# Kernel optimization log

Hardware: AMD Instinct MI355X
Metric: run time of the kernel (lower is better)

Reference implementation:

```python
import jax, jax.numpy as jnp
import numpy as np

N = 100000       # nodes
E = 1600000      # edges
D_IN = 128       # input_dim
D_H = 64         # embedding_dim
N_LAYERS = 3     # total GCNConv layers (conv1 + 2 hidden)
DROP_P = 0.5     # F.dropout default (training=True by default in functional form)


def setup_inputs() -> dict:
    key = jax.random.key(0)
    ks = jax.random.split(key, 8)
    x = jax.random.normal(ks[0], (N, D_IN), dtype=jnp.float32)
    edge_index = jax.random.randint(ks[1], (2, E), 0, N, dtype=jnp.int32)
    edge_attr = jax.random.uniform(ks[2], (E,), dtype=jnp.float32)
    # learned parameters (glorot-ish scale, zero bias like PyG defaults)
    W1 = jax.random.normal(ks[3], (D_IN, D_H), dtype=jnp.float32) / np.sqrt(D_IN).astype(np.float32)
    b1 = jnp.zeros((D_H,), jnp.float32)
    Wh = jax.random.normal(ks[4], (N_LAYERS - 1, D_H, D_H), dtype=jnp.float32) / np.sqrt(D_H).astype(np.float32)
    bh = jnp.zeros((N_LAYERS - 1, D_H), jnp.float32)
    lin_W = jax.random.normal(ks[5], (D_H, 1), dtype=jnp.float32) / np.sqrt(D_H).astype(np.float32)
    lin_b = jnp.zeros((1,), jnp.float32)
    return dict(x=x, edge_index=edge_index, edge_attr=edge_attr,
                W1=W1, b1=b1, Wh=Wh, bh=bh, lin_W=lin_W, lin_b=lin_b)


def _gcn_norm(edge_index, edge_weight):
    # PyG gcn_norm: add self-loops with weight 1, symmetric deg^-1/2 normalization.
    loop = jnp.arange(N, dtype=edge_index.dtype)
    src = jnp.concatenate([edge_index[0], loop])   # message sources
    dst = jnp.concatenate([edge_index[1], loop])   # aggregate at targets
    w = jnp.concatenate([edge_weight, jnp.ones((N,), edge_weight.dtype)])
    deg = jax.ops.segment_sum(w, dst, num_segments=N)
    dinv = jnp.where(deg > 0, jax.lax.rsqrt(deg), 0.0)
    norm = dinv[src] * w * dinv[dst]               # [E+N]
    return src, dst, norm


def _gcn_conv(h, W, b, src, dst, norm):
    h = h @ W                                       # [N, D]
    msg = h[src] * norm[:, None]                    # gather + scale, [E+N, D]
    out = jax.ops.segment_sum(msg, dst, num_segments=N)  # scatter-add
    return out + b


def _dropout(h, key, p=DROP_P):
    keep = jax.random.bernoulli(key, 1.0 - p, h.shape)
    return jnp.where(keep, h / (1.0 - p), 0.0)


def reference(x, edge_index, edge_attr, W1, b1, Wh, bh, lin_W, lin_b):
    src, dst, norm = _gcn_norm(edge_index, edge_attr)
    dk = jax.random.split(jax.random.key(42), N_LAYERS)
    h = _dropout(jax.nn.elu(_gcn_conv(x, W1, b1, src, dst, norm)), dk[0])
    for i in range(N_LAYERS - 1):
        h = _dropout(jax.nn.elu(_gcn_conv(h, Wh[i], bh[i], src, dst, norm)), dk[i + 1])
    return h @ lin_W + lin_b                        # [N, 1]
```

## Files before the change

kernel.cpp:

```cpp
#include <hip/hip_runtime.h>
#include <hip/hip_fp16.h>
#include <stdint.h>

#define NNODES 100000
#define NEDGES 1600000
#define DINPUT 128
#define DH 64
#define NELEM (NNODES * DH)
#define CAP 48
#define SCAN_B 1024
#define SCAN_NB ((NNODES + SCAN_B - 1) / SCAN_B)

#define G_GEMM (NNODES / 32)
#define G_EDGE (NEDGES / 256)
#define G_GATH (NNODES / 16)

__host__ __device__ __forceinline__ void tf2x32(uint32_t k0, uint32_t k1,
                                                uint32_t x0, uint32_t x1,
                                                uint32_t* o0, uint32_t* o1) {
  uint32_t k2 = k0 ^ k1 ^ 0x1BD11BDAu;
  x0 += k0; x1 += k1;
#define TF_ROT(r) { x0 += x1; x1 = (x1 << (r)) | (x1 >> (32 - (r))); x1 ^= x0; }
  TF_ROT(13) TF_ROT(15) TF_ROT(26) TF_ROT(6)
  x0 += k1; x1 += k2 + 1u;
  TF_ROT(17) TF_ROT(29) TF_ROT(16) TF_ROT(24)
  x0 += k2; x1 += k0 + 2u;
  TF_ROT(13) TF_ROT(15) TF_ROT(26) TF_ROT(6)
  x0 += k0; x1 += k1 + 3u;
  TF_ROT(17) TF_ROT(29) TF_ROT(16) TF_ROT(24)
  x0 += k1; x1 += k2 + 4u;
  TF_ROT(13) TF_ROT(15) TF_ROT(26) TF_ROT(6)
  x0 += k2; x1 += k0 + 5u;
#undef TF_ROT
  *o0 = x0; *o1 = x1;
}

__device__ __forceinline__ float4 h4_load(const int2* hp, size_t idx) {
  int2 r = hp[idx];
  __half2 a = *reinterpret_cast<__half2*>(&r.x);
  __half2 b = *reinterpret_cast<__half2*>(&r.y);
  float2 fa = __half22float2(a);
  float2 fb = __half22float2(b);
  return float4{fa.x, fa.y, fb.x, fb.y};
}
__device__ __forceinline__ int2 h4_pack(float4 v) {
  __half2 a = __floats2half2_rn(v.x, v.y);
  __half2 b = __floats2half2_rn(v.z, v.w);
  int2 r;
  r.x = *reinterpret_cast<int*>(&a);
  r.y = *reinterpret_cast<int*>(&b);
  return r;
}

__global__ void k_zero(int* cnt) {
  int n = blockIdx.x * 256 + threadIdx.x;
  if (n < NNODES) cnt[n] = 0;
}

__global__ __launch_bounds__(256) void k_fill_gemm(
    const int* __restrict__ src, const int* __restrict__ dst,
    const float* __restrict__ w, int* cnt, int2* __restrict__ cp,
    const float* __restrict__ x, const float* __restrict__ W1,
    __half* __restrict__ B, int gemm_only) {
  __shared__ float Wt[DH][DINPUT + 4];
  __shared__ float4 rows4[32][DINPUT / 4];
  int t = threadIdx.x;
  int bid = blockIdx.x;
  int g, r;
  if (gemm_only) { g = bid; r = 2; } else { g = bid / 3; r = bid % 3; }
  if (r == 2) {
    for (int i = t; i < DINPUT * DH; i += 256) {
      int k = i >> 6, d = i & 63;
      Wt[d][k] = W1[i];
    }
    int n0 = g * 32;
    const float4* hv = (const float4*)x;
    for (int i = t; i < 32 * (DINPUT / 4); i += 256) {
      int rr = i >> 5, kk = i & 31;
      rows4[rr][kk] = hv[(size_t)(n0 + rr) * (DINPUT / 4) + kk];
    }
    __syncthreads();
    int d = t & 63;
    int wv = t >> 6;
    float acc[8] = {0.f, 0.f, 0.f, 0.f, 0.f, 0.f, 0.f, 0.f};
    const float4* wt4 = (const float4*)&Wt[d][0];
#pragma unroll 4
    for (int kq = 0; kq < DINPUT / 4; ++kq) {
      float4 wq = wt4[kq];
#pragma unroll
      for (int rr = 0; rr < 8; ++rr) {
        float4 hq = rows4[wv * 8 + rr][kq];
        acc[rr] += hq.x * wq.x + hq.y * wq.y + hq.z * wq.z + hq.w * wq.w;
      }
    }
#pragma unroll
    for (int rr = 0; rr < 8; ++rr)
      B[(size_t)(n0 + wv * 8 + rr) * DH + d] = __float2half_rn(acc[rr]);
  } else {
    int f = g * 2 + r;
    int e = f * 256 + t;
    int s = src[e], d = dst[e];
    int slot = atomicAdd(&cnt[d], 1);
    if (slot < CAP) cp[(size_t)d * CAP + slot] = int2{s, __float_as_int(w[e])};
  }
}

__global__ void k_hist(const int* __restrict__ dst, int* cnt) {
  int e = blockIdx.x * 256 + threadIdx.x;
  if (e < NEDGES) atomicAdd(&cnt[dst[e]], 1);
}

__global__ __launch_bounds__(1024) void k_scan1(const int* __restrict__ cnt,
                                                int* __restrict__ lpre,
                                                int* __restrict__ bsum) {
  __shared__ int ps[SCAN_B];
  int t = threadIdx.x;
  int n = blockIdx.x * SCAN_B + t;
  int v = (n < NNODES) ? cnt[n] : 0;
  ps[t] = v;
  __syncthreads();
  for (int off = 1; off < SCAN_B; off <<= 1) {
    int u = (t >= off) ? ps[t - off] : 0;
    __syncthreads();
    ps[t] += u;
    __syncthreads();
  }
  if (n < NNODES) lpre[n] = ps[t] - v;
  if (t == SCAN_B - 1) bsum[blockIdx.x] = ps[t];
}

__global__ __launch_bounds__(128) void k_scan2(int* bsum) {
  __shared__ int ps[128];
  int t = threadIdx.x;
  int v = (t < SCAN_NB) ? bsum[t] : 0;
  ps[t] = v;
  __syncthreads();
  for (int off = 1; off < 128; off <<= 1) {
    int u = (t >= off) ? ps[t - off] : 0;
    __syncthreads();
    ps[t] += u;
    __syncthreads();
  }
  if (t < SCAN_NB) bsum[t] = ps[t] - v;
}

__global__ __launch_bounds__(1024) void k_scan3(const int* __restrict__ bsum,
                                                int* __restrict__ lpre_rowptr,
                                                int* __restrict__ wptr) {
  int t = threadIdx.x;
  int n = blockIdx.x * SCAN_B + t;
  if (n < NNODES) {
    int r = lpre_rowptr[n] + bsum[blockIdx.x];
    lpre_rowptr[n] = r;
    wptr[n] = r;
  }
  if (n == 0) lpre_rowptr[NNODES] = NEDGES;
}

__global__ void k_fill_compact(const int* __restrict__ src, const int* __restrict__ dst,
                               const float* __restrict__ w, int* wptr,
                               int2* __restrict__ cp) {
  int e = blockIdx.x * 256 + threadIdx.x;
  if (e < NEDGES) {
    int s = src[e], d = dst[e];
    int slot = atomicAdd(&wptr[d], 1);
    cp[slot] = int2{s, __float_as_int(w[e])};
  }
}

template <int PADDED>
__global__ __launch_bounds__(256) void k_degrow(const int* __restrict__ rowptr,
                                                const int* __restrict__ cnt,
                                                const int2* __restrict__ cp,
                                                float* __restrict__ dinv) {
  int g = blockIdx.x * 16 + (threadIdx.x >> 4);
  int sl = threadIdx.x & 15;
  int beg = PADDED ? g * CAP : rowptr[g];
  int num = PADDED ? min(cnt[g], CAP) : rowptr[g + 1] - beg;
  float s = 0.0f;
  for (int i = sl; i < num; i += 16) s += __int_as_float(cp[beg + i].y);
  s += __shfl_xor(s, 1);
  s += __shfl_xor(s, 2);
  s += __shfl_xor(s, 4);
  s += __shfl_xor(s, 8);
  if (sl == 0) dinv[g] = 1.0f / sqrtf(1.0f + s);
}

template <int MODE, int PADDED>
__global__ __launch_bounds__(256) void k_gg(
    const __half* __restrict__ h2, const int* __restrict__ rowptr,
    const int* __restrict__ cnt, const int2* __restrict__ cpair,
    const float* __restrict__ dinv, const float* __restrict__ bias,
    const float* __restrict__ Wn, const float* __restrict__ lw,
    const float* __restrict__ lb, void* __restrict__ outp,
    uint32_t k0, uint32_t k1) {
  __shared__ float4 Ws4[DH * 16];
  __shared__ float4 hs4[16 * 17];
  int t = threadIdx.x;
  int g = blockIdx.x * 16 + (t >> 4);
  int sl = t & 15;
  int n = t >> 4;
  const int2* h4 = (const int2*)h2;

  if (MODE == 0) {
    const float4* wv = (const float4*)Wn;
    for (int i = t; i < DH * 16; i += 256) Ws4[i] = wv[i];
  }

  float dg = dinv[g];
  float4 self = h4_load(h4, (size_t)g * 16 + sl);
  float4 acc = {0.f, 0.f, 0.f, 0.f};

  int beg = PADDED ? g * CAP : rowptr[g];
  int end = beg + (PADDED ? min(cnt[g], CAP) : rowptr[g + 1] - beg);

  int e = beg;
  for (; e + 8 <= end; e += 8) {
    int2 p0 = cpair[e + 0], p1 = cpair[e + 1], p2 = cpair[e + 2], p3 = cpair[e + 3];
    int2 p4 = cpair[e + 4], p5 = cpair[e + 5], p6 = cpair[e + 6], p7 = cpair[e + 7];
    float d0 = dinv[p0.x], d1 = dinv[p1.x], d2 = dinv[p2.x], d3 = dinv[p3.x];
    float d4 = dinv[p4.x], d5 = dinv[p5.x], d6 = dinv[p6.x], d7 = dinv[p7.x];
    float4 v0 = h4_load(h4, (size_t)p0.x * 16 + sl);
    float4 v1 = h4_load(h4, (size_t)p1.x * 16 + sl);
    float4 v2 = h4_load(h4, (size_t)p2.x * 16 + sl);
    float4 v3 = h4_load(h4, (size_t)p3.x * 16 + sl);
    float4 v4 = h4_load(h4, (size_t)p4.x * 16 + sl);
    float4 v5 = h4_load(h4, (size_t)p5.x * 16 + sl);
    float4 v6 = h4_load(h4, (size_t)p6.x * 16 + sl);
    float4 v7 = h4_load(h4, (size_t)p7.x * 16 + sl);
    float w0 = d0 * __int_as_float(p0.y), w1 = d1 * __int_as_float(p1.y);
    float w2 = d2 * __int_as_float(p2.y), w3 = d3 * __int_as_float(p3.y);
    float w4 = d4 * __int_as_float(p4.y), w5 = d5 * __int_as_float(p5.y);
    float w6 = d6 * __int_as_float(p6.y), w7 = d7 * __int_as_float(p7.y);
    acc.x += v0.x * w0 + v1.x * w1 + v2.x * w2 + v3.x * w3
           + v4.x * w4 + v5.x * w5 + v6.x * w6 + v7.x * w7;
    acc.y += v0.y * w0 + v1.y * w1 + v2.y * w2 + v3.y * w3
           + v4.y * w4 + v5.y * w5 + v6.y * w6 + v7.y * w7;
    acc.z += v0.z * w0 + v1.z * w1 + v2.z * w2 + v3.z * w3
           + v4.z * w4 + v5.z * w5 + v6.z * w6 + v7.z * w7;
    acc.w += v0.w * w0 + v1.w * w1 + v2.w * w2 + v3.w * w3
           + v4.w * w4 + v5.w * w5 + v6.w * w6 + v7.w * w7;
  }
  for (; e < end; ++e) {
    int2 p = cpair[e];
    float nm = dinv[p.x] * __int_as_float(p.y);
    float4 v = h4_load(h4, (size_t)p.x * 16 + sl);
    acc.x += v.x * nm;
    acc.y += v.y * nm;
    acc.z += v.z * nm;
    acc.w += v.w * nm;
  }

  const float4 bv = ((const float4*)bias)[sl];
  acc.x = dg * (acc.x + dg * self.x) + bv.x;
  acc.y = dg * (acc.y + dg * self.y) + bv.y;
  acc.z = dg * (acc.z + dg * self.z) + bv.z;
  acc.w = dg * (acc.w + dg * self.w) + bv.w;

  acc.x = (acc.x > 0.0f) ? acc.x : expm1f(acc.x);
  acc.y = (acc.y > 0.0f) ? acc.y : expm1f(acc.y);
  acc.z = (acc.z > 0.0f) ? acc.z : expm1f(acc.z);
  acc.w = (acc.w > 0.0f) ? acc.w : expm1f(acc.w);

  uint32_t base = (uint32_t)g * 64u + (uint32_t)sl * 4u;
  uint32_t o0, o1;
  tf2x32(k0, k1, 0u, base + 0u, &o0, &o1);
  acc.x = (((o0 ^ o1) >> 31) == 0u) ? 2.0f * acc.x : 0.0f;
  tf2x32(k0, k1, 0u, base + 1u, &o0, &o1);
  acc.y = (((o0 ^ o1) >> 31) == 0u) ? 2.0f * acc.y : 0.0f;
  tf2x32(k0, k1, 0u, base + 2u, &o0, &o1);
  acc.z = (((o0 ^ o1) >> 31) == 0u) ? 2.0f * acc.z : 0.0f;
  tf2x32(k0, k1, 0u, base + 3u, &o0, &o1);
  acc.w = (((o0 ^ o1) >> 31) == 0u) ? 2.0f * acc.w : 0.0f;

  if (MODE == 1) {
    const float4 lv = ((const float4*)lw)[sl];
    float dot = acc.x * lv.x + acc.y * lv.y + acc.z * lv.z + acc.w * lv.w;
    dot += __shfl_xor(dot, 1);
    dot += __shfl_xor(dot, 2);
    dot += __shfl_xor(dot, 4);
    dot += __shfl_xor(dot, 8);
    if (sl == 0) ((float*)outp)[g] = dot + lb[0];
  } else {
    hs4[n * 17 + sl] = acc;
    __syncthreads();
    float4 o = {0.f, 0.f, 0.f, 0.f};
#pragma unroll
    for (int dq = 0; dq < 16; ++dq) {
      float4 hq = hs4[n * 17 + dq];
      float4 w0 = Ws4[(dq * 4 + 0) * 16 + sl];
      float4 w1 = Ws4[(dq * 4 + 1) * 16 + sl];
      float4 w2 = Ws4[(dq * 4 + 2) * 16 + sl];
      float4 w3 = Ws4[(dq * 4 + 3) * 16 + sl];
      o.x += hq.x * w0.x + hq.y * w1.x + hq.z * w2.x + hq.w * w3.x;
      o.y += hq.x * w0.y + hq.y * w1.y + hq.z * w2.y + hq.w * w3.y;
      o.z += hq.x * w0.z + hq.y * w1.z + hq.z * w2.z + hq.w * w3.z;
      o.w += hq.x * w0.w + hq.y * w1.w + hq.z * w2.w + hq.w * w3.w;
    }
    ((int2*)outp)[(size_t)g * 16 + sl] = h4_pack(o);
  }
}

extern "C" void kernel_launch(void* const* d_in, const int* in_sizes, int n_in,
                              void* d_out, int out_size, void* d_ws, size_t ws_size,
                              hipStream_t stream) {
  const float* x   = (const float*)d_in[0];
  const int*   ei  = (const int*)d_in[1];
  const float* ew  = (const float*)d_in[2];
  const float* W1  = (const float*)d_in[3];
  const float* b1  = (const float*)d_in[4];
  const float* Wh  = (const float*)d_in[5];
  const float* bh  = (const float*)d_in[6];
  const float* lw  = (const float*)d_in[7];
  const float* lb  = (const float*)d_in[8];
  float* out = (float*)d_out;

  const int* src = ei;
  const int* dst = ei + NEDGES;

  const size_t capE = (size_t)NNODES * CAP;
  const size_t needPadded =
      (size_t)NELEM * 2 * 2 + capE * 8 +
      ((size_t)NNODES * 3 + 1 + SCAN_NB) * 4;
  const bool padded = ws_size >= needPadded;
  const size_t nSlots = padded ? capE : (size_t)NEDGES;

  __half* A     = (__half*)d_ws;
  __half* B     = A + (size_t)NELEM;
  int2*  cpair  = (int2*)(B + (size_t)NELEM);
  float* dinv   = (float*)(cpair + nSlots);
  int*   cnt    = (int*)(dinv + (size_t)NNODES);
  int*   rowptr = cnt + (size_t)NNODES;
  int*   wptr   = rowptr + (size_t)NNODES + 1;
  int*   bsum   = wptr + (size_t)NNODES;

  uint32_t dk[3][2];
  for (uint32_t i = 0; i < 3; ++i) tf2x32(0u, 42u, 0u, i, &dk[i][0], &dk[i][1]);

  const int gN = (NNODES + 255) / 256;
  const float* Wh0 = Wh;
  const float* Wh1 = Wh + (size_t)DH * DH;

  if (padded) {
    k_zero<<<gN, 256, 0, stream>>>(cnt);
    k_fill_gemm<<<3 * G_GEMM, 256, 0, stream>>>(src, dst, ew, cnt, cpair,
                                                x, W1, B, 0);
    k_degrow<1><<<G_GATH, 256, 0, stream>>>(rowptr, cnt, cpair, dinv);

    k_gg<0, 1><<<G_GATH, 256, 0, stream>>>(B, rowptr, cnt, cpair, dinv, b1,
                                           Wh0, lw, lb, A, dk[0][0], dk[0][1]);
    k_gg<0, 1><<<G_GATH, 256, 0, stream>>>(A, rowptr, cnt, cpair, dinv, bh,
                                           Wh1, lw, lb, B, dk[1][0], dk[1][1]);
    k_gg<1, 1><<<G_GATH, 256, 0, stream>>>(B, rowptr, cnt, cpair, dinv, bh + DH,
                                           nullptr, lw, lb, out, dk[2][0], dk[2][1]);
  } else {
    k_zero<<<gN, 256, 0, stream>>>(cnt);
    k_hist<<<G_EDGE, 256, 0, stream>>>(dst, cnt);
    k_scan1<<<SCAN_NB, SCAN_B, 0, stream>>>(cnt, rowptr, bsum);
    k_scan2<<<1, 128, 0, stream>>>(bsum);
    k_scan3<<<SCAN_NB, SCAN_B, 0, stream>>>(bsum, rowptr, wptr);
    k_fill_compact<<<G_EDGE, 256, 0, stream>>>(src, dst, ew, wptr, cpair);
    k_degrow<0><<<G_GATH, 256, 0, stream>>>(rowptr, cnt, cpair, dinv);
    k_fill_gemm<<<G_GEMM, 256, 0, stream>>>(src, dst, ew, cnt, nullptr,
                                            x, W1, B, 1);

    k_gg<0, 0><<<G_GATH, 256, 0, stream>>>(B, rowptr, cnt, cpair, dinv, b1,
                                           Wh0, lw, lb, A, dk[0][0], dk[0][1]);
    k_gg<0, 0><<<G_GATH, 256, 0, stream>>>(A, rowptr, cnt, cpair, dinv, bh,
                                           Wh1, lw, lb, B, dk[1][0], dk[1][1]);
    k_gg<1, 0><<<G_GATH, 256, 0, stream>>>(B, rowptr, cnt, cpair, dinv, bh + DH,
                                           nullptr, lw, lb, out, dk[2][0], dk[2][1]);
  }
}
```

Before: 260.6 us.

## Gather 8 halves per lane with 32 nodes per block; nontemporal edge fill

The gather kernel now assigns 8 lanes per node, each loading 16-byte int4 chunks of fp16 features, so a block processes 32 nodes instead of 16. This halves the grid, and the 64x64 dense transform is remapped so each thread handles two nodes. The fill kernel also uses nontemporal loads for the edge arrays and a nontemporal packed 64-bit store for adjacency pairs. Wider loads cut instruction count per gathered row, but each gathered row is split across fewer lanes and per-thread register use rises.

```diff
diff --git a/kernel.cpp b/kernel.cpp
--- a/kernel.cpp
+++ b/kernel.cpp
@@ -14,6 +14,7 @@
 #define G_GEMM (NNODES / 32)
 #define G_EDGE (NEDGES / 256)
 #define G_GATH (NNODES / 16)
+#define G_GATH2 (NNODES / 32)
 
 __host__ __device__ __forceinline__ void tf2x32(uint32_t k0, uint32_t k1,
                                                 uint32_t x0, uint32_t x1,
@@ -35,13 +36,13 @@
   *o0 = x0; *o1 = x1;
 }
 
-__device__ __forceinline__ float4 h4_load(const int2* hp, size_t idx) {
-  int2 r = hp[idx];
-  __half2 a = *reinterpret_cast<__half2*>(&r.x);
-  __half2 b = *reinterpret_cast<__half2*>(&r.y);
-  float2 fa = __half22float2(a);
-  float2 fb = __half22float2(b);
-  return float4{fa.x, fa.y, fb.x, fb.y};
+__device__ __forceinline__ void h8_unpack(int4 r, float* f) {
+  __half2* h = reinterpret_cast<__half2*>(&r);
+  float2 a;
+  a = __half22float2(h[0]); f[0] = a.x; f[1] = a.y;
+  a = __half22float2(h[1]); f[2] = a.x; f[3] = a.y;
+  a = __half22float2(h[2]); f[4] = a.x; f[5] = a.y;
+  a = __half22float2(h[3]); f[6] = a.x; f[7] = a.y;
 }
 __device__ __forceinline__ int2 h4_pack(float4 v) {
   __half2 a = __floats2half2_rn(v.x, v.y);
@@ -99,9 +100,14 @@
   } else {
     int f = g * 2 + r;
     int e = f * 256 + t;
-    int s = src[e], d = dst[e];
+    int s  = __builtin_nontemporal_load(src + e);
+    int d  = __builtin_nontemporal_load(dst + e);
+    float wv = __builtin_nontemporal_load(w + e);
     int slot = atomicAdd(&cnt[d], 1);
-    if (slot < CAP) cp[(size_t)d * CAP + slot] = int2{s, __float_as_int(w[e])};
+    if (slot < CAP) {
+      long long pv = ((long long)__float_as_int(wv) << 32) | (unsigned)s;
+      __builtin_nontemporal_store(pv, (long long*)(cp + (size_t)d * CAP + slot));
+    }
   }
 }
 
@@ -195,12 +201,12 @@
     const float* __restrict__ lb, void* __restrict__ outp,
     uint32_t k0, uint32_t k1) {
   __shared__ float4 Ws4[DH * 16];
-  __shared__ float4 hs4[16 * 17];
-  int t = threadIdx.x;
-  int g = blockIdx.x * 16 + (t >> 4);
-  int sl = t & 15;
-  int n = t >> 4;
-  const int2* h4 = (const int2*)h2;
+  __shared__ float4 hs4[32 * 17];
+  int t = threadIdx.x;
+  int gl = t >> 3;
+  int g = blockIdx.x * 32 + gl;
+  int sl = t & 7;
+  const int4* h8 = (const int4*)h2;
 
   if (MODE == 0) {
     const float4* wv = (const float4*)Wn;
@@ -208,8 +214,9 @@
   }
 
   float dg = dinv[g];
-  float4 self = h4_load(h4, (size_t)g * 16 + sl);
-  float4 acc = {0.f, 0.f, 0.f, 0.f};
+  float self[8];
+  h8_unpack(h8[(size_t)g * 8 + sl], self);
+  float acc[8] = {0.f, 0.f, 0.f, 0.f, 0.f, 0.f, 0.f, 0.f};
 
   int beg = PADDED ? g * CAP : rowptr[g];
   int end = beg + (PADDED ? min(cnt[g], CAP) : rowptr[g + 1] - beg);
@@ -218,86 +225,83 @@
   for (; e + 8 <= end; e += 8) {
     int2 p0 = cpair[e + 0], p1 = cpair[e + 1], p2 = cpair[e + 2], p3 = cpair[e + 3];
     int2 p4 = cpair[e + 4], p5 = cpair[e + 5], p6 = cpair[e + 6], p7 = cpair[e + 7];
-    float d0 = dinv[p0.x], d1 = dinv[p1.x], d2 = dinv[p2.x], d3 = dinv[p3.x];
-    float d4 = dinv[p4.x], d5 = dinv[p5.x], d6 = dinv[p6.x], d7 = dinv[p7.x];
-    float4 v0 = h4_load(h4, (size_t)p0.x * 16 + sl);
-    float4 v1 = h4_load(h4, (size_t)p1.x * 16 + sl);
-    float4 v2 = h4_load(h4, (size_t)p2.x * 16 + sl);
-    float4 v3 = h4_load(h4, (size_t)p3.x * 16 + sl);
-    float4 v4 = h4_load(h4, (size_t)p4.x * 16 + sl);
-    float4 v5 = h4_load(h4, (size_t)p5.x * 16 + sl);
-    float4 v6 = h4_load(h4, (size_t)p6.x * 16 + sl);
-    float4 v7 = h4_load(h4, (size_t)p7.x * 16 + sl);
-    float w0 = d0 * __int_as_float(p0.y), w1 = d1 * __int_as_float(p1.y);
-    float w2 = d2 * __int_as_float(p2.y), w3 = d3 * __int_as_float(p3.y);
-    float w4 = d4 * __int_as_float(p4.y), w5 = d5 * __int_as_float(p5.y);
-    float w6 = d6 * __int_as_float(p6.y), w7 = d7 * __int_as_float(p7.y);
-    acc.x += v0.x * w0 + v1.x * w1 + v2.x * w2 + v3.x * w3
-           + v4.x * w4 + v5.x * w5 + v6.x * w6 + v7.x * w7;
-    acc.y += v0.y * w0 + v1.y * w1 + v2.y * w2 + v3.y * w3
-           + v4.y * w4 + v5.y * w5 + v6.y * w6 + v7.y * w7;
-    acc.z += v0.z * w0 + v1.z * w1 + v2.z * w2 + v3.z * w3
-           + v4.z * w4 + v5.z * w5 + v6.z * w6 + v7.z * w7;
-    acc.w += v0.w * w0 + v1.w * w1 + v2.w * w2 + v3.w * w3
-           + v4.w * w4 + v5.w * w5 + v6.w * w6 + v7.w * w7;
+    int4 r0 = h8[(size_t)p0.x * 8 + sl];
+    int4 r1 = h8[(size_t)p1.x * 8 + sl];
+    int4 r2 = h8[(size_t)p2.x * 8 + sl];
+    int4 r3 = h8[(size_t)p3.x * 8 + sl];
+    int4 r4 = h8[(size_t)p4.x * 8 + sl];
+    int4 r5 = h8[(size_t)p5.x * 8 + sl];
+    int4 r6 = h8[(size_t)p6.x * 8 + sl];
+    int4 r7 = h8[(size_t)p7.x * 8 + sl];
+    float w0 = dinv[p0.x] * __int_as_float(p0.y);
+    float w1 = dinv[p1.x] * __int_as_float(p1.y);
+    float w2 = dinv[p2.x] * __int_as_float(p2.y);
+    float w3 = dinv[p3.x] * __int_as_float(p3.y);
+    float w4 = dinv[p4.x] * __int_as_float(p4.y);
+    float w5 = dinv[p5.x] * __int_as_float(p5.y);
+    float w6 = dinv[p6.x] * __int_as_float(p6.y);
+    float w7 = dinv[p7.x] * __int_as_float(p7.y);
+    float v[8];
+#define ACC8(R, W) { h8_unpack(R, v); _Pragma("unroll") \
+    for (int j = 0; j < 8; ++j) acc[j] += v[j] * (W); }
+    ACC8(r0, w0) ACC8(r1, w1) ACC8(r2, w2) ACC8(r3, w3)
+    ACC8(r4, w4) ACC8(r5, w5) ACC8(r6, w6) ACC8(r7, w7)
   }
   for (; e < end; ++e) {
     int2 p = cpair[e];
     float nm = dinv[p.x] * __int_as_float(p.y);
-    float4 v = h4_load(h4, (size_t)p.x * 16 + sl);
-    acc.x += v.x * nm;
-    acc.y += v.y * nm;
-    acc.z += v.z * nm;
-    acc.w += v.w * nm;
-  }
-
-  const float4 bv = ((const float4*)bias)[sl];
-  acc.x = dg * (acc.x + dg * self.x) + bv.x;
-  acc.y = dg * (acc.y + dg * self.y) + bv.y;
-  acc.z = dg * (acc.z + dg * self.z) + bv.z;
-  acc.w = dg * (acc.w + dg * self.w) + bv.w;
-
-  acc.x = (acc.x > 0.0f) ? acc.x : expm1f(acc.x);
-  acc.y = (acc.y > 0.0f) ? acc.y : expm1f(acc.y);
-  acc.z = (acc.z > 0.0f) ? acc.z : expm1f(acc.z);
-  acc.w = (acc.w > 0.0f) ? acc.w : expm1f(acc.w);
-
-  uint32_t base = (uint32_t)g * 64u + (uint32_t)sl * 4u;
-  uint32_t o0, o1;
-  tf2x32(k0, k1, 0u, base + 0u, &o0, &o1);
-  acc.x = (((o0 ^ o1) >> 31) == 0u) ? 2.0f * acc.x : 0.0f;
-  tf2x32(k0, k1, 0u, base + 1u, &o0, &o1);
-  acc.y = (((o0 ^ o1) >> 31) == 0u) ? 2.0f * acc.y : 0.0f;
-  tf2x32(k0, k1, 0u, base + 2u, &o0, &o1);
-  acc.z = (((o0 ^ o1) >> 31) == 0u) ? 2.0f * acc.z : 0.0f;
-  tf2x32(k0, k1, 0u, base + 3u, &o0, &o1);
-  acc.w = (((o0 ^ o1) >> 31) == 0u) ? 2.0f * acc.w : 0.0f;
+    float v[8];
+    h8_unpack(h8[(size_t)p.x * 8 + sl], v);
+#pragma unroll
+    for (int j = 0; j < 8; ++j) acc[j] += v[j] * nm;
+  }
+#undef ACC8
+
+  const float4* b4 = (const float4*)bias;
+  float4 ba = b4[sl * 2 + 0], bb = b4[sl * 2 + 1];
+  float bv[8] = {ba.x, ba.y, ba.z, ba.w, bb.x, bb.y, bb.z, bb.w};
+  uint32_t base = (uint32_t)g * 64u + (uint32_t)sl * 8u;
+#pragma unroll
+  for (int j = 0; j < 8; ++j) {
+    float h = dg * (acc[j] + dg * self[j]) + bv[j];
+    h = (h > 0.0f) ? h : expm1f(h);
+    uint32_t o0, o1;
+    tf2x32(k0, k1, 0u, base + (uint32_t)j, &o0, &o1);
+    acc[j] = (((o0 ^ o1) >> 31) == 0u) ? 2.0f * h : 0.0f;
+  }
 
   if (MODE == 1) {
-    const float4 lv = ((const float4*)lw)[sl];
-    float dot = acc.x * lv.x + acc.y * lv.y + acc.z * lv.z + acc.w * lv.w;
+    const float4* l4 = (const float4*)lw;
+    float4 la = l4[sl * 2 + 0], lbv = l4[sl * 2 + 1];
+    float dot = acc[0] * la.x + acc[1] * la.y + acc[2] * la.z + acc[3] * la.w
+              + acc[4] * lbv.x + acc[5] * lbv.y + acc[6] * lbv.z + acc[7] * lbv.w;
     dot += __shfl_xor(dot, 1);
     dot += __shfl_xor(dot, 2);
     dot += __shfl_xor(dot, 4);
-    dot += __shfl_xor(dot, 8);
     if (sl == 0) ((float*)outp)[g] = dot + lb[0];
   } else {
-    hs4[n * 17 + sl] = acc;
-    __syncthreads();
-    float4 o = {0.f, 0.f, 0.f, 0.f};
-#pragma unroll
-    for (int dq = 0; dq < 16; ++dq) {
-      float4 hq = hs4[n * 17 + dq];
-      float4 w0 = Ws4[(dq * 4 + 0) * 16 + sl];
-      float4 w1 = Ws4[(dq * 4 + 1) * 16 + sl];
-      float4 w2 = Ws4[(dq * 4 + 2) * 16 + sl];
-      float4 w3 = Ws4[(dq * 4 + 3) * 16 + sl];
-      o.x += hq.x * w0.x + hq.y * w1.x + hq.z * w2.x + hq.w * w3.x;
-      o.y += hq.x * w0.y + hq.y * w1.y + hq.z * w2.y + hq.w * w3.y;
-      o.z += hq.x * w0.z + hq.y * w1.z + hq.z * w2.z + hq.w * w3.z;
-      o.w += hq.x * w0.w + hq.y * w1.w + hq.z * w2.w + hq.w * w3.w;
-    }
-    ((int2*)outp)[(size_t)g * 16 + sl] = h4_pack(o);
+    hs4[gl * 17 + sl * 2 + 0] = float4{acc[0], acc[1], acc[2], acc[3]};
+    hs4[gl * 17 + sl * 2 + 1] = float4{acc[4], acc[5], acc[6], acc[7]};
+    __syncthreads();
+    int n2 = t >> 4, sl2 = t & 15;
+#pragma unroll
+    for (int it = 0; it < 2; ++it) {
+      int node = n2 + it * 16;
+      float4 o = {0.f, 0.f, 0.f, 0.f};
+#pragma unroll
+      for (int dq = 0; dq < 16; ++dq) {
+        float4 hq = hs4[node * 17 + dq];
+        float4 w0 = Ws4[(dq * 4 + 0) * 16 + sl2];
+        float4 w1 = Ws4[(dq * 4 + 1) * 16 + sl2];
+        float4 w2 = Ws4[(dq * 4 + 2) * 16 + sl2];
+        float4 w3 = Ws4[(dq * 4 + 3) * 16 + sl2];
+        o.x += hq.x * w0.x + hq.y * w1.x + hq.z * w2.x + hq.w * w3.x;
+        o.y += hq.x * w0.y + hq.y * w1.y + hq.z * w2.y + hq.w * w3.y;
+        o.z += hq.x * w0.z + hq.y * w1.z + hq.z * w2.z + hq.w * w3.z;
+        o.w += hq.x * w0.w + hq.y * w1.w + hq.z * w2.w + hq.w * w3.w;
+      }
+      ((int2*)outp)[((size_t)blockIdx.x * 32 + node) * 16 + sl2] = h4_pack(o);
+    }
   }
 }
 
@@ -347,12 +351,12 @@
                                                 x, W1, B, 0);
     k_degrow<1><<<G_GATH, 256, 0, stream>>>(rowptr, cnt, cpair, dinv);
 
-    k_gg<0, 1><<<G_GATH, 256, 0, stream>>>(B, rowptr, cnt, cpair, dinv, b1,
-                                           Wh0, lw, lb, A, dk[0][0], dk[0][1]);
-    k_gg<0, 1><<<G_GATH, 256, 0, stream>>>(A, rowptr, cnt, cpair, dinv, bh,
-                                           Wh1, lw, lb, B, dk[1][0], dk[1][1]);
-    k_gg<1, 1><<<G_GATH, 256, 0, stream>>>(B, rowptr, cnt, cpair, dinv, bh + DH,
-                                           nullptr, lw, lb, out, dk[2][0], dk[2][1]);
+    k_gg<0, 1><<<G_GATH2, 256, 0, stream>>>(B, rowptr, cnt, cpair, dinv, b1,
+                                            Wh0, lw, lb, A, dk[0][0], dk[0][1]);
+    k_gg<0, 1><<<G_GATH2, 256, 0, stream>>>(A, rowptr, cnt, cpair, dinv, bh,
+                                            Wh1, lw, lb, B, dk[1][0], dk[1][1]);
+    k_gg<1, 1><<<G_GATH2, 256, 0, stream>>>(B, rowptr, cnt, cpair, dinv, bh + DH,
+                                            nullptr, lw, lb, out, dk[2][0], dk[2][1]);
   } else {
     k_zero<<<gN, 256, 0, stream>>>(cnt);
     k_hist<<<G_EDGE, 256, 0, stream>>>(dst, cnt);
@@ -364,11 +368,11 @@
     k_fill_gemm<<<G_GEMM, 256, 0, stream>>>(src, dst, ew, cnt, nullptr,
                                             x, W1, B, 1);
 
-    k_gg<0, 0><<<G_GATH, 256, 0, stream>>>(B, rowptr, cnt, cpair, dinv, b1,
-                                           Wh0, lw, lb, A, dk[0][0], dk[0][1]);
-    k_gg<0, 0><<<G_GATH, 256, 0, stream>>>(A, rowptr, cnt, cpair, dinv, bh,
-                                           Wh1, lw, lb, B, dk[1][0], dk[1][1]);
-    k_gg<1, 0><<<G_GATH, 256, 0, stream>>>(B, rowptr, cnt, cpair, dinv, bh + DH,
-                                           nullptr, lw, lb, out, dk[2][0], dk[2][1]);
-  }
-}
+    k_gg<0, 0><<<G_GATH2, 256, 0, stream>>>(B, rowptr, cnt, cpair, dinv, b1,
+                                            Wh0, lw, lb, A, dk[0][0], dk[0][1]);
+    k_gg<0, 0><<<G_GATH2, 256, 0, stream>>>(A, rowptr, cnt, cpair, dinv, bh,
+                                            Wh1, lw, lb, B, dk[1][0], dk[1][1]);
+    k_gg<1, 0><<<G_GATH2, 256, 0, stream>>>(B, rowptr, cnt, cpair, dinv, bh + DH,
+                                            nullptr, lw, lb, out, dk[2][0], dk[2][1]);
+  }
+}
```

After: 336.8 us. 1.29x slower.
